# Kernel optimization log

Measured on AMD Instinct MI355X. Metric: run time of the kernel, lower is better.

Reference implementation:

```python
import jax, jax.numpy as jnp
import numpy as np

N_NODES = 100000
N_EDGES = 1600000
D_IN = 16
D_HID = 32   # 2 * out_channels
D_OUT = 16


def gcn_conv(h, src, dst, W, b, num_nodes):
    """PyG-style GCNConv: x' = D^{-1/2} (A+I) D^{-1/2} (x W) + b.
    src/dst already include self-loops."""
    h = h @ W                                   # [N, F_out] linear transform first
    deg = jnp.zeros((num_nodes,), h.dtype).at[dst].add(1.0)
    dinv = jax.lax.rsqrt(jnp.maximum(deg, 1.0))  # deg >= 1 due to self-loops
    norm = dinv[src] * dinv[dst]                # [E+N]
    msg = h[src] * norm[:, None]                # edge gather (memory-bound)
    out = jax.ops.segment_sum(msg, dst, num_segments=num_nodes)
    return out + b


def setup_inputs() -> dict:
    key = jax.random.key(0)
    k1, k2, k3, k4 = jax.random.split(key, 4)
    x = jnp.arange(N_NODES, dtype=jnp.int32)
    edge_index = jax.random.randint(k1, (2, N_EDGES), 0, N_NODES, dtype=jnp.int32)
    emb = jax.random.normal(k2, (N_NODES, D_IN), dtype=jnp.float32)
    W1 = jax.random.normal(k3, (D_IN, D_HID), dtype=jnp.float32) * (1.0 / np.sqrt(D_IN))
    b1 = jnp.zeros((D_HID,), jnp.float32)
    W2 = jax.random.normal(k4, (D_HID, D_OUT), dtype=jnp.float32) * (1.0 / np.sqrt(D_HID))
    b2 = jnp.zeros((D_OUT,), jnp.float32)
    return {"x": x, "edge_index": edge_index, "emb": emb,
            "W1": W1, "b1": b1, "W2": W2, "b2": b2}


def reference(x, edge_index, emb, W1, b1, W2, b2):
    num_nodes = emb.shape[0]
    # add self-loops once; reused by both conv layers
    loops = jnp.arange(num_nodes, dtype=edge_index.dtype)
    src = jnp.concatenate([edge_index[0], loops])
    dst = jnp.concatenate([edge_index[1], loops])

    h = emb[x]                                  # embedding lookup
    h = jax.nn.relu(gcn_conv(h, src, dst, W1, b1, num_nodes))
    # dropout is identity in eval mode (reference baseline)
    out = gcn_conv(h, src, dst, W2, b2, num_nodes)
    return out
```

## Files before the change

### kernel.cpp

```cpp
#include <hip/hip_runtime.h>


#define BS   256
#define BSBIG 1024
#define NBLK 256
#define BINSHIFT 8
#define BIN  256
#define MAXBINS 512
#define BINCAP 4608
#define BINSTRIDE 4608

union H2 { int i; _Float16 h[2]; };

__global__ __launch_bounds__(BSBIG) void k_scatter(
    const int* __restrict__ src, const int* __restrict__ dst,
    int E, int NBINS, int* __restrict__ gbin, int* __restrict__ packed) {
    __shared__ int h[MAXBINS];
    __shared__ int cur[MAXBINS];
    int t = threadIdx.x;
    for (int i = t; i < NBINS; i += BSBIG) h[i] = 0;
    __syncthreads();
    int E4 = E >> 2;
    const int4* d4 = (const int4*)dst;
    const int4* s4 = (const int4*)src;
    for (int i = blockIdx.x * BSBIG + t; i < E4; i += NBLK * BSBIG) {
        int4 d = d4[i];
        atomicAdd(&h[d.x >> BINSHIFT], 1);
        atomicAdd(&h[d.y >> BINSHIFT], 1);
        atomicAdd(&h[d.z >> BINSHIFT], 1);
        atomicAdd(&h[d.w >> BINSHIFT], 1);
    }
    if (blockIdx.x == 0 && t < (E & 3))
        atomicAdd(&h[dst[(E4 << 2) + t] >> BINSHIFT], 1);
    __syncthreads();
    for (int i = t; i < NBINS; i += BSBIG)
        cur[i] = i * BINSTRIDE + atomicAdd(&gbin[i], h[i]);
    __syncthreads();
    for (int i = blockIdx.x * BSBIG + t; i < E4; i += NBLK * BSBIG) {
        int4 s = s4[i];
        int4 d = d4[i];
        int p0 = atomicAdd(&cur[d.x >> BINSHIFT], 1);
        packed[p0] = s.x | ((d.x & (BIN - 1)) << 18);
        int p1 = atomicAdd(&cur[d.y >> BINSHIFT], 1);
        packed[p1] = s.y | ((d.y & (BIN - 1)) << 18);
        int p2 = atomicAdd(&cur[d.z >> BINSHIFT], 1);
        packed[p2] = s.z | ((d.z & (BIN - 1)) << 18);
        int p3 = atomicAdd(&cur[d.w >> BINSHIFT], 1);
        packed[p3] = s.w | ((d.w & (BIN - 1)) << 18);
    }
    if (blockIdx.x == 0 && t < (E & 3)) {
        int e = (E4 << 2) + t;
        int d = dst[e];
        int p = atomicAdd(&cur[d >> BINSHIFT], 1);
        packed[p] = src[e] | ((d & (BIN - 1)) << 18);
    }
}

__global__ void k_binsort(const int* __restrict__ packed,
                          const int* __restrict__ gbin,
                          int NBINS, int N, int E,
                          const int* __restrict__ x, const float* __restrict__ emb,
                          const float* __restrict__ W1,
                          int* __restrict__ row_start, float* __restrict__ dinv,
                          int* __restrict__ col, _Float16* __restrict__ sig1) {
    __shared__ int buf[BINCAP];
    __shared__ int ldeg[BIN];
    __shared__ int lrs[BIN];
    __shared__ int cur[BIN];
    __shared__ int ssc[BS];
    __shared__ int bofl[MAXBINS];
    __shared__ float sW[512];
    int b = blockIdx.x;
    int t = threadIdx.x;
    int node0 = b << BINSHIFT;
    int PERs = (NBINS + BS - 1) / BS;
    int loc[4];
    int sbase = t * PERs;
    int ssum = 0;
    for (int j = 0; j < PERs && j < 4; j++) {
        int idx = sbase + j;
        int v = (idx < NBINS) ? gbin[idx] : 0;
        loc[j] = ssum;
        ssum += v;
    }
    ssc[t] = ssum;
    __syncthreads();
    for (int off = 1; off < BS; off <<= 1) {
        int add = (t >= off) ? ssc[t - off] : 0;
        __syncthreads();
        ssc[t] += add;
        __syncthreads();
    }
    {
        int ex = ssc[t] - ssum;
        for (int j = 0; j < PERs && j < 4; j++) {
            int idx = sbase + j;
            if (idx < NBINS) bofl[idx] = ex + loc[j];
        }
    }
    __syncthreads();
    int e0 = bofl[b];
    int cnt = gbin[b];
    int p0 = b * BINSTRIDE;
    bool fits = (cnt <= BINCAP);
    if (b == 0 && t == 0) row_start[N] = E;
    sW[t] = W1[t];
    sW[t + 256] = W1[t + 256];
    ldeg[t] = 0;
    if (fits)
        for (int i = t; i < cnt; i += BS) buf[i] = packed[p0 + i];
    __syncthreads();
    for (int i = t; i < cnt; i += BS) {
        int v = fits ? buf[i] : packed[p0 + i];
        atomicAdd(&ldeg[((unsigned)v >> 18) & (BIN - 1)], 1);
    }
    __syncthreads();
    lrs[t] = ldeg[t];
    __syncthreads();
    for (int off = 1; off < BIN; off <<= 1) {
        int add = (t >= off) ? lrs[t - off] : 0;
        __syncthreads();
        lrs[t] += add;
        __syncthreads();
    }
    int myDeg = ldeg[t];
    int ex = lrs[t] - myDeg;
    cur[t] = ex;
    int n = node0 + t;
    float di = rsqrtf((float)(myDeg + 1));
    if (n < N) {
        row_start[n] = e0 + ex;
        dinv[n] = di;
    }
    __syncthreads();
    for (int i = t; i < cnt; i += BS) {
        int v = fits ? buf[i] : packed[p0 + i];
        int pos = atomicAdd(&cur[((unsigned)v >> 18) & (BIN - 1)], 1);
        col[e0 + pos] = v & 0x3FFFF;
    }
    if (n < N) {
        const float4* er = (const float4*)(emb + (size_t)x[n] * 16);
        float4 ra = er[0], rb = er[1], rc = er[2], rd = er[3];
        float ev[16] = {ra.x, ra.y, ra.z, ra.w, rb.x, rb.y, rb.z, rb.w,
                        rc.x, rc.y, rc.z, rc.w, rd.x, rd.y, rd.z, rd.w};
        int4* s1o = (int4*)sig1;
        #pragma unroll
        for (int cq = 0; cq < 4; cq++) {
            H2 pk[4];
            #pragma unroll
            for (int dw = 0; dw < 4; dw++) {
                int c = cq * 8 + dw * 2;
                float acc0 = 0.f, acc1 = 0.f;
                #pragma unroll
                for (int k = 0; k < 16; k++) {
                    acc0 += ev[k] * sW[k * 32 + c];
                    acc1 += ev[k] * sW[k * 32 + c + 1];
                }
                pk[dw].h[0] = (_Float16)(acc0 * di);
                pk[dw].h[1] = (_Float16)(acc1 * di);
            }
            int4 pv;
            pv.x = pk[0].i; pv.y = pk[1].i; pv.z = pk[2].i; pv.w = pk[3].i;
            s1o[(size_t)n * 4 + cq] = pv;
        }
    }
}

__global__ __launch_bounds__(BS) void k_agg1mm2(
    const _Float16* __restrict__ sig1, const int* __restrict__ row_start,
    const float* __restrict__ dinv, const int* __restrict__ col,
    const float* __restrict__ b1, const float* __restrict__ W2,
    int N, _Float16* __restrict__ sig2) {
    __shared__ float hbuf[4][4][36];
    int t = threadIdx.x;
    int lane = t & 63;
    int wid = t >> 6;
    int g  = lane >> 4;
    int cd = lane & 15;
    int n = blockIdx.x * 16 + wid * 4 + g;
    int nld = (n < N) ? n : N - 1;
    int rs = row_start[nld];
    int re = row_start[nld + 1];
    int dn = (n < N) ? (re - rs) : 0;
    int dnm1 = (dn > 0) ? dn - 1 : 0;
    int dm = dn;
    dm = max(dm, __shfl_xor(dm, 16));
    dm = max(dm, __shfl_xor(dm, 32));
    float w2c[32];
    #pragma unroll
    for (int k = 0; k < 32; k++) w2c[k] = W2[k * 16 + cd];
    const int* s1i = (const int*)sig1;
    float a0 = 0.f, a1 = 0.f;
    int iters = (dm + 7) >> 3;
    int slot = cd & 7;
    int bidx = lane & 48;
    int colv = 0;
    if (iters > 0) {
        int idx = slot; if (idx > dnm1) idx = dnm1;
        colv = col[rs + idx];
    }
    for (int it = 0; it < iters; it++) {
        int e = it << 3;
        int coln = 0;
        if (it + 1 < iters) {
            int idx = e + 8 + slot; if (idx > dnm1) idx = dnm1;
            coln = col[rs + idx];
        }
        int s0 = __shfl(colv, bidx + 0);
        int s1 = __shfl(colv, bidx + 1);
        int s2 = __shfl(colv, bidx + 2);
        int s3 = __shfl(colv, bidx + 3);
        int s4 = __shfl(colv, bidx + 4);
        int s5 = __shfl(colv, bidx + 5);
        int s6 = __shfl(colv, bidx + 6);
        int s7 = __shfl(colv, bidx + 7);
        int u0 = s1i[s0 * 16 + cd];
        int u1 = s1i[s1 * 16 + cd];
        int u2 = s1i[s2 * 16 + cd];
        int u3 = s1i[s3 * 16 + cd];
        int u4 = s1i[s4 * 16 + cd];
        int u5 = s1i[s5 * 16 + cd];
        int u6 = s1i[s6 * 16 + cd];
        int u7 = s1i[s7 * 16 + cd];
        u0 = (e + 0 < dn) ? u0 : 0;
        u1 = (e + 1 < dn) ? u1 : 0;
        u2 = (e + 2 < dn) ? u2 : 0;
        u3 = (e + 3 < dn) ? u3 : 0;
        u4 = (e + 4 < dn) ? u4 : 0;
        u5 = (e + 5 < dn) ? u5 : 0;
        u6 = (e + 6 < dn) ? u6 : 0;
        u7 = (e + 7 < dn) ? u7 : 0;
        H2 p0, p1, p2, p3;
        p0.i = u0; p1.i = u1; p2.i = u2; p3.i = u3;
        a0 += ((float)p0.h[0] + (float)p1.h[0]) + ((float)p2.h[0] + (float)p3.h[0]);
        a1 += ((float)p0.h[1] + (float)p1.h[1]) + ((float)p2.h[1] + (float)p3.h[1]);
        p0.i = u4; p1.i = u5; p2.i = u6; p3.i = u7;
        a0 += ((float)p0.h[0] + (float)p1.h[0]) + ((float)p2.h[0] + (float)p3.h[0]);
        a1 += ((float)p0.h[1] + (float)p1.h[1]) + ((float)p2.h[1] + (float)p3.h[1]);
        colv = coln;
    }
    {
        H2 p; p.i = s1i[nld * 16 + cd];
        a0 += (float)p.h[0];
        a1 += (float)p.h[1];
    }
    float di = dinv[nld];
    float2 b = ((const float2*)b1)[cd];
    float h0 = fmaxf(a0 * di + b.x, 0.f);
    float h1 = fmaxf(a1 * di + b.y, 0.f);
    float* hb = hbuf[wid][g];
    *(float2*)&hb[2 * cd] = make_float2(h0, h1);
    float a = 0.f;
    #pragma unroll
    for (int k = 0; k < 32; k += 4) {
        float4 hv = *(const float4*)&hb[k];
        a = fmaf(hv.x, w2c[k],     a);
        a = fmaf(hv.y, w2c[k + 1], a);
        a = fmaf(hv.z, w2c[k + 2], a);
        a = fmaf(hv.w, w2c[k + 3], a);
    }
    if (n < N) sig2[(size_t)n * 16 + cd] = (_Float16)(a * di);
}

__global__ __launch_bounds__(BS) void k_agg2(
    const _Float16* __restrict__ sig2, const int* __restrict__ row_start,
    const float* __restrict__ dinv, const int* __restrict__ col,
    const float* __restrict__ b2, int N, float* __restrict__ out) {
    int t = threadIdx.x;
    int lane = t & 63;
    int g  = lane >> 4;
    int e2 = (lane >> 3) & 1;
    int cd = lane & 7;
    int n = blockIdx.x * 16 + (t >> 6) * 4 + g;
    int nld = (n < N) ? n : N - 1;
    int rs = row_start[nld];
    int re = row_start[nld + 1];
    int dn = (n < N) ? (re - rs) : 0;
    int dnm1 = (dn > 0) ? dn - 1 : 0;
    int dm = dn;
    dm = max(dm, __shfl_xor(dm, 16));
    dm = max(dm, __shfl_xor(dm, 32));
    const int* s2i = (const int*)sig2;
    float a0 = 0.f, a1 = 0.f;
    int iters = (dm + 15) >> 4;
    int slot = lane & 15;
    int bidx = lane & 48;
    int colv = 0;
    if (iters > 0) {
        int idx = slot; if (idx > dnm1) idx = dnm1;
        colv = col[rs + idx];
    }
    for (int it = 0; it < iters; it++) {
        int e = it << 4;
        int coln = 0;
        if (it + 1 < iters) {
            int idx = e + 16 + slot; if (idx > dnm1) idx = dnm1;
            coln = col[rs + idx];
        }
        #pragma unroll
        for (int j = 0; j < 8; j++) {
            int sl = 2 * j + e2;
            int sv = __shfl(colv, bidx + sl);
            int u = s2i[sv * 8 + cd];
            u = (e + sl < dn) ? u : 0;
            H2 p; p.i = u;
            a0 += (float)p.h[0];
            a1 += (float)p.h[1];
        }
        colv = coln;
    }
    a0 += __shfl_xor(a0, 8);
    a1 += __shfl_xor(a1, 8);
    {
        H2 p; p.i = s2i[nld * 8 + cd];
        a0 += (float)p.h[0];
        a1 += (float)p.h[1];
    }
    if (n < N && e2 == 0) {
        float di = dinv[nld];
        float2 b = ((const float2*)b2)[cd];
        float2 o;
        o.x = a0 * di + b.x;
        o.y = a1 * di + b.y;
        ((float2*)out)[(size_t)n * 8 + cd] = o;
    }
}

extern "C" void kernel_launch(void* const* d_in, const int* in_sizes, int n_in,
                              void* d_out, int out_size, void* d_ws, size_t ws_size,
                              hipStream_t stream) {
    const int*   x   = (const int*)d_in[0];
    const int*   ei  = (const int*)d_in[1];
    const float* emb = (const float*)d_in[2];
    const float* W1  = (const float*)d_in[3];
    const float* b1  = (const float*)d_in[4];
    const float* W2  = (const float*)d_in[5];
    const float* b2  = (const float*)d_in[6];
    float* out = (float*)d_out;

    const int N = in_sizes[0];
    const int E = in_sizes[1] / 2;
    const int* srcp = ei;
    const int* dstp = ei + E;
    const int NBINS = (N + BIN - 1) >> BINSHIFT;

    auto al = [](size_t b) { return (b + 255) & ~size_t(255); };
    char* w = (char*)d_ws;
    auto carve = [&](size_t bytes) {
        void* p = (void*)w;
        w += al(bytes);
        return p;
    };
    int*   row_start = (int*)carve((size_t)(N + 1) * 4);
    float* dinv      = (float*)carve((size_t)N * 4);
    int*   col       = (int*)carve((size_t)(E + 256) * 4);
    int*   gbin      = (int*)carve((size_t)NBINS * 4);
    int*   packed    = (int*)carve((size_t)NBINS * BINSTRIDE * 4);
    _Float16* sig1   = (_Float16*)carve((size_t)N * 32 * 2);
    _Float16* sig2   = (_Float16*)carve((size_t)N * 16 * 2);
    (void)ws_size; (void)n_in; (void)out_size;

    hipMemsetAsync(gbin, 0, (size_t)NBINS * 4, stream);
    k_scatter<<<NBLK, BSBIG, 0, stream>>>(srcp, dstp, E, NBINS, gbin, packed);
    k_binsort<<<NBINS, BS, 0, stream>>>(packed, gbin, NBINS, N, E,
                                        x, emb, W1, row_start, dinv, col, sig1);

    int gA = (N + 15) / 16;
    k_agg1mm2<<<gA, BS, 0, stream>>>(sig1, row_start, dinv, col, b1, W2, N, sig2);
    k_agg2<<<gA, BS, 0, stream>>>(sig2, row_start, dinv, col, b2, N, out);
}
```

Baseline: 150.5 us.

## Halve bin size, replace block-wide scans with wave shuffles, split node transform

Bins shrink from 256 to 128 nodes, which doubles the number of binsort blocks and cuts per-block shared memory. Each block now finds its edge offset by summing the preceding bin counts with a wavefront shuffle reduction, replacing the full shared-memory scan over all bins. The per-node degree scan also uses wave shuffles. The first-layer transform is split across two threads per node, each computing half the output channels. The cost is redundant global reads of gbin that grow with the block index, and bins are more likely to exceed the smaller buffer capacity and fall back to global reads.

Result: no change. 148.2 us (-1.5%).

```diff
diff --git a/kernel.cpp b/kernel.cpp
--- a/kernel.cpp
+++ b/kernel.cpp
@@ -4,11 +4,11 @@
 #define BS   256
 #define BSBIG 1024
 #define NBLK 256
-#define BINSHIFT 8
-#define BIN  256
-#define MAXBINS 512
-#define BINCAP 4608
-#define BINSTRIDE 4608
+#define BINSHIFT 7
+#define BIN  128
+#define MAXBINS 1024
+#define BINCAP 2560
+#define BINSTRIDE 2560
 
 union H2 { int i; _Float16 h[2]; };
 
@@ -65,48 +65,29 @@
                           int* __restrict__ col, _Float16* __restrict__ sig1) {
     __shared__ int buf[BINCAP];
     __shared__ int ldeg[BIN];
-    __shared__ int lrs[BIN];
     __shared__ int cur[BIN];
-    __shared__ int ssc[BS];
-    __shared__ int bofl[MAXBINS];
     __shared__ float sW[512];
+    __shared__ int redw[4];
+    __shared__ int wtot[2];
     int b = blockIdx.x;
     int t = threadIdx.x;
+    int lane = t & 63;
+    int wv = t >> 6;
     int node0 = b << BINSHIFT;
-    int PERs = (NBINS + BS - 1) / BS;
-    int loc[4];
-    int sbase = t * PERs;
-    int ssum = 0;
-    for (int j = 0; j < PERs && j < 4; j++) {
-        int idx = sbase + j;
-        int v = (idx < NBINS) ? gbin[idx] : 0;
-        loc[j] = ssum;
-        ssum += v;
-    }
-    ssc[t] = ssum;
-    __syncthreads();
-    for (int off = 1; off < BS; off <<= 1) {
-        int add = (t >= off) ? ssc[t - off] : 0;
-        __syncthreads();
-        ssc[t] += add;
-        __syncthreads();
-    }
-    {
-        int ex = ssc[t] - ssum;
-        for (int j = 0; j < PERs && j < 4; j++) {
-            int idx = sbase + j;
-            if (idx < NBINS) bofl[idx] = ex + loc[j];
-        }
-    }
-    __syncthreads();
-    int e0 = bofl[b];
+    int ps = 0;
+    for (int i = t; i < b; i += BS) ps += gbin[i];
+    #pragma unroll
+    for (int off = 1; off < 64; off <<= 1) ps += __shfl_xor(ps, off);
+    if (lane == 0) redw[wv] = ps;
+    sW[t] = W1[t];
+    sW[t + 256] = W1[t + 256];
+    if (t < BIN) ldeg[t] = 0;
+    if (b == 0 && t == 0) row_start[N] = E;
+    __syncthreads();
+    int e0 = redw[0] + redw[1] + redw[2] + redw[3];
     int cnt = gbin[b];
     int p0 = b * BINSTRIDE;
     bool fits = (cnt <= BINCAP);
-    if (b == 0 && t == 0) row_start[N] = E;
-    sW[t] = W1[t];
-    sW[t + 256] = W1[t + 256];
-    ldeg[t] = 0;
     if (fits)
         for (int i = t; i < cnt; i += BS) buf[i] = packed[p0 + i];
     __syncthreads();
@@ -115,22 +96,27 @@
         atomicAdd(&ldeg[((unsigned)v >> 18) & (BIN - 1)], 1);
     }
     __syncthreads();
-    lrs[t] = ldeg[t];
-    __syncthreads();
-    for (int off = 1; off < BIN; off <<= 1) {
-        int add = (t >= off) ? lrs[t - off] : 0;
-        __syncthreads();
-        lrs[t] += add;
-        __syncthreads();
-    }
-    int myDeg = ldeg[t];
-    int ex = lrs[t] - myDeg;
-    cur[t] = ex;
-    int n = node0 + t;
-    float di = rsqrtf((float)(myDeg + 1));
-    if (n < N) {
-        row_start[n] = e0 + ex;
-        dinv[n] = di;
+    int myDeg = 0, inc = 0;
+    if (t < BIN) {
+        myDeg = ldeg[t];
+        inc = myDeg;
+        #pragma unroll
+        for (int off = 1; off < 64; off <<= 1) {
+            int tmp = __shfl_up(inc, off);
+            if (lane >= off) inc += tmp;
+        }
+        if (lane == 63) wtot[wv] = inc;
+    }
+    __syncthreads();
+    if (t < BIN) {
+        int pre = (wv == 1) ? wtot[0] : 0;
+        int ex = (inc - myDeg) + pre;
+        cur[t] = ex;
+        int n = node0 + t;
+        if (n < N) {
+            row_start[n] = e0 + ex;
+            dinv[n] = rsqrtf((float)(myDeg + 1));
+        }
     }
     __syncthreads();
     for (int i = t; i < cnt; i += BS) {
@@ -138,14 +124,19 @@
         int pos = atomicAdd(&cur[((unsigned)v >> 18) & (BIN - 1)], 1);
         col[e0 + pos] = v & 0x3FFFF;
     }
+    int nl = t & (BIN - 1);
+    int half = t >> 7;
+    int n = node0 + nl;
     if (n < N) {
+        float di = rsqrtf((float)(ldeg[nl] + 1));
         const float4* er = (const float4*)(emb + (size_t)x[n] * 16);
         float4 ra = er[0], rb = er[1], rc = er[2], rd = er[3];
         float ev[16] = {ra.x, ra.y, ra.z, ra.w, rb.x, rb.y, rb.z, rb.w,
                         rc.x, rc.y, rc.z, rc.w, rd.x, rd.y, rd.z, rd.w};
         int4* s1o = (int4*)sig1;
         #pragma unroll
-        for (int cq = 0; cq < 4; cq++) {
+        for (int cq2 = 0; cq2 < 2; cq2++) {
+            int cq = half * 2 + cq2;
             H2 pk[4];
             #pragma unroll
             for (int dw = 0; dw < 4; dw++) {
```
